# Optimization experiments

Hardware: AMD Instinct MI355X
Metric: run time of the kernel (lower is better)

Reference implementation:

```python
import jax, jax.numpy as jnp
import numpy as np

EPS = 1e-5

def _conv1x1(x, w, b=None):
    # x: (B, Cin, H, W), w: (Cout, Cin) -> (B, Cout, H, W)
    y = jnp.einsum('bchw,oc->bohw', x, w)
    if b is not None:
        y = y + b[None, :, None, None]
    return y

def setup_inputs() -> dict:
    key = jax.random.key(0)
    ks = jax.random.split(key, 14)
    B, C, I = 4, 256, 128
    Ha = Wa = 64
    Hd = Wd = 128
    s = 0.05
    return {
        'detect':  jax.random.normal(ks[0], (B, C, Hd, Wd), jnp.float32),
        'aim':     jax.random.normal(ks[1], (B, C, Ha, Wa), jnp.float32),
        'g_w':     jax.random.normal(ks[2], (I, C), jnp.float32) * s,
        'g_b':     jax.random.normal(ks[3], (I,), jnp.float32) * s,
        'theta_w': jax.random.normal(ks[4], (I, C), jnp.float32) * s,
        'theta_b': jax.random.normal(ks[5], (I,), jnp.float32) * s,
        'phi_w':   jax.random.normal(ks[6], (I, C), jnp.float32) * s,
        'phi_b':   jax.random.normal(ks[7], (I,), jnp.float32) * s,
        'q_w':     jax.random.normal(ks[8], (C, I), jnp.float32) * s,
        'q_b':     jax.random.normal(ks[9], (C,), jnp.float32) * s,
        'bn_gamma': jax.random.normal(ks[10], (C,), jnp.float32),
        'bn_beta':  jax.random.normal(ks[11], (C,), jnp.float32),
        'bn_mean':  jax.random.normal(ks[12], (C,), jnp.float32),
        'bn_var':   jax.random.uniform(ks[13], (C,), jnp.float32) + 0.5,
    }

def reference(detect, aim, g_w, g_b, theta_w, theta_b, phi_w, phi_b,
              q_w, q_b, bn_gamma, bn_beta, bn_mean, bn_var):
    B, C, Hd, Wd = detect.shape
    _, _, Ha, Wa = aim.shape
    Na = Ha * Wa
    Nd = Hd * Wd
    I = g_w.shape[0]

    # 1x1 conv projections, flattened to token sequences
    a_g   = _conv1x1(aim, g_w, g_b).reshape(B, I, Na)        # g(aim)
    th_a  = _conv1x1(aim, theta_w, theta_b).reshape(B, I, Na)
    ph_d  = _conv1x1(detect, phi_w, phi_b).reshape(B, I, Nd)
    # (d_x = g(detect) is dead code in the original forward; omitted)

    # f = theta_x @ phi_x : (B, Na, Nd); permuted -> (B, Nd, Na); N = Na
    f = jnp.einsum('bia,bid->bad', th_a, ph_d)               # (B, Na, Nd)
    inv_n = jnp.float32(1.0 / Na)
    # non_det = (f^T / Na) @ a_x : (B, Nd, I) -> permute -> (B, I, Nd)
    non = jnp.einsum('bad,bia->bid', f * inv_n, a_g)         # (B, I, Nd)
    non = non.reshape(B, I, Hd, Wd)

    # Q: 1x1 conv (I -> C) + BatchNorm (inference mode, running stats)
    y = _conv1x1(non, q_w, q_b)
    inv_std = jax.lax.rsqrt(bn_var + EPS)
    y = (y - bn_mean[None, :, None, None]) * (bn_gamma * inv_std)[None, :, None, None] \
        + bn_beta[None, :, None, None]

    return y + detect
```

## Files before the change

kernel.cpp:

```cpp
#include <hip/hip_runtime.h>

constexpr int BB   = 4;
constexpr int CCH  = 256;
constexpr int IDIM = 128;
constexpr int NAa  = 4096;
constexpr int NDd  = 16384;
constexpr int PAD  = 320;
constexpr float NAinv = 1.0f / 4096.0f;

typedef __bf16 bf16x8 __attribute__((ext_vector_type(8)));
typedef float  f32x4  __attribute__((ext_vector_type(4)));

__device__ inline unsigned short f2bfu(float f) {
    unsigned u = __float_as_uint(f);
    u += 0x7FFFu + ((u >> 16) & 1u);
    return (unsigned short)(u >> 16);
}

__global__ __launch_bounds__(256) void k_front(const float* __restrict__ aim,
                                               unsigned short* __restrict__ Abf,
                                               float* __restrict__ r,
                                               const float* __restrict__ qw,
                                               const float* __restrict__ gw,
                                               const float* __restrict__ gb,
                                               const float* __restrict__ thw,
                                               const float* __restrict__ thb,
                                               const float* __restrict__ phw,
                                               const float* __restrict__ phb,
                                               unsigned short* __restrict__ Ph,
                                               unsigned short* __restrict__ Rt) {
    __shared__ float red[256];
    const int t = threadIdx.x;
    if (blockIdx.x < BB * CCH) {
        const int row = blockIdx.x;
        const float* src = aim + (long)row * NAa;
        unsigned short* dst = Abf + (long)row * NAa;
        float s = 0.f;
        #pragma unroll
        for (int j = 0; j < 4; ++j) {
            const int e = (j * 256 + t) * 4;
            float4 v = *(const float4*)(src + e);
            s += v.x + v.y + v.z + v.w;
            ushort4 o; o.x = f2bfu(v.x); o.y = f2bfu(v.y); o.z = f2bfu(v.z); o.w = f2bfu(v.w);
            *(ushort4*)(dst + e) = o;
        }
        red[t] = s; __syncthreads();
        for (int st = 128; st > 0; st >>= 1) { if (t < st) red[t] += red[t + st]; __syncthreads(); }
        if (t == 0) r[row] = red[0];
    } else {
        const int idx = (blockIdx.x - BB * CCH) * 256 + t;
        if (idx < CCH * PAD) {
            const int o = idx / PAD, c = idx - o * PAD;
            float acc = 0.f;
            if (c <= 256) {
                for (int i = 0; i < IDIM; ++i)
                    acc += qw[o * IDIM + i] * ((c < 256) ? gw[i * CCH + c] : gb[i]);
            }
            Ph[idx] = f2bfu(acc);
        } else {
            const int id2 = idx - CCH * PAD;
            const int c2 = id2 / PAD, k = id2 - c2 * PAD;
            float acc = 0.f;
            if (k <= 256 && c2 <= 256) {
                for (int i = 0; i < IDIM; ++i) {
                    const float av = (k < 256) ? thw[i * CCH + k] : thb[i];
                    const float bv = (c2 < 256) ? phw[i * CCH + c2] : phb[i];
                    acc += av * bv;
                }
            }
            Rt[id2] = f2bfu(acc);
        }
    }
}

__global__ __launch_bounds__(64) void k_S(const unsigned short* __restrict__ Abf,
                                          float* __restrict__ Spart) {
    const int z = blockIdx.z, b = z >> 3, chunk = z & 7;
    const unsigned short* A = Abf + (long)b * CCH * NAa;
    const int lane = threadIdx.x, quad = lane >> 4, l16 = lane & 15;
    const int mb = blockIdx.y * 64, nb = blockIdx.x * 64;
    const int kb = chunk * 512;
    f32x4 acc[4][4] = {};
    for (int ks = 0; ks < 16; ++ks) {
        const int k = kb + ks * 32 + quad * 8;
        bf16x8 af[4], bfr[4];
        #pragma unroll
        for (int i = 0; i < 4; ++i) af[i]  = *(const bf16x8*)(A + (long)(mb + i * 16 + l16) * NAa + k);
        #pragma unroll
        for (int j = 0; j < 4; ++j) bfr[j] = *(const bf16x8*)(A + (long)(nb + j * 16 + l16) * NAa + k);
        #pragma unroll
        for (int i = 0; i < 4; ++i)
            #pragma unroll
            for (int j = 0; j < 4; ++j)
                acc[i][j] = __builtin_amdgcn_mfma_f32_16x16x32_bf16(af[i], bfr[j], acc[i][j], 0, 0, 0);
    }
    float* o = Spart + (long)z * CCH * CCH;
    #pragma unroll
    for (int i = 0; i < 4; ++i)
        #pragma unroll
        for (int j = 0; j < 4; ++j)
            #pragma unroll
            for (int reg = 0; reg < 4; ++reg)
                o[(long)(mb + i * 16 + quad * 4 + reg) * CCH + nb + j * 16 + l16] = acc[i][j][reg];
}

__global__ __launch_bounds__(256) void k_red(const float* __restrict__ Spart,
                                             const float* __restrict__ r,
                                             unsigned short* __restrict__ Shat) {
    const int b = blockIdx.y;
    const int idx = blockIdx.x * 256 + threadIdx.x;
    const int k = idx / PAD, n = idx - k * PAD;
    float v = 0.f;
    if (k < 256 && n < 256) {
        #pragma unroll
        for (int p = 0; p < 8; ++p)
            v += Spart[(long)(b * 8 + p) * CCH * CCH + k * CCH + n];
    } else if (k == 256 && n < 256) v = r[b * CCH + n];
    else if (n == 256 && k < 256)   v = r[b * CCH + k];
    else if (k == 256 && n == 256)  v = 4096.0f;
    Shat[(long)b * PAD * PAD + idx] = f2bfu(v);
}

__global__ __launch_bounds__(256) void k_t(const unsigned short* __restrict__ Ph,
                                           const unsigned short* __restrict__ Sh,
                                           const unsigned short* __restrict__ Rt,
                                           const float* __restrict__ qb,
                                           const float* __restrict__ gamma,
                                           const float* __restrict__ beta,
                                           const float* __restrict__ mean,
                                           const float* __restrict__ var,
                                           unsigned short* __restrict__ W5u,
                                           float* __restrict__ b5) {
    const int b = blockIdx.y;
    const int m0 = blockIdx.x * 64;
    const unsigned short* S = Sh + (long)b * PAD * PAD;
    const int t = threadIdx.x, w = t >> 6, lane = t & 63, quad = lane >> 4, l16 = lane & 15;
    __shared__ __align__(16) unsigned short Tl[64][328];

    {
        f32x4 a1[4][5] = {};
        for (int kt = 0; kt < PAD; kt += 32) {
            bf16x8 af[4], bfr[5];
            #pragma unroll
            for (int i = 0; i < 4; ++i)
                af[i] = *(const bf16x8*)(Ph + (long)(m0 + i * 16 + l16) * PAD + kt + quad * 8);
            #pragma unroll
            for (int j = 0; j < 5; ++j)
                bfr[j] = *(const bf16x8*)(S + (long)(w * 80 + j * 16 + l16) * PAD + kt + quad * 8);
            #pragma unroll
            for (int i = 0; i < 4; ++i)
                #pragma unroll
                for (int j = 0; j < 5; ++j)
                    a1[i][j] = __builtin_amdgcn_mfma_f32_16x16x32_bf16(af[i], bfr[j], a1[i][j], 0, 0, 0);
        }
        #pragma unroll
        for (int i = 0; i < 4; ++i)
            #pragma unroll
            for (int j = 0; j < 5; ++j)
                #pragma unroll
                for (int reg = 0; reg < 4; ++reg)
                    Tl[i * 16 + quad * 4 + reg][w * 80 + j * 16 + l16] = f2bfu(a1[i][j][reg]);
    }
    __syncthreads();

    for (int pass = 0; pass < 2; ++pass) {
        if (pass == 1 && w != 0) break;
        const int n0 = (pass == 0) ? w * 64 : 256;
        f32x4 acc[4][4] = {};
        for (int kt = 0; kt < PAD; kt += 32) {
            bf16x8 af[4], bfr[4];
            #pragma unroll
            for (int i = 0; i < 4; ++i)
                af[i] = *(const bf16x8*)&Tl[i * 16 + l16][kt + quad * 8];
            #pragma unroll
            for (int j = 0; j < 4; ++j)
                bfr[j] = *(const bf16x8*)(Rt + (long)(n0 + j * 16 + l16) * PAD + kt + quad * 8);
            #pragma unroll
            for (int i = 0; i < 4; ++i)
                #pragma unroll
                for (int j = 0; j < 4; ++j)
                    acc[i][j] = __builtin_amdgcn_mfma_f32_16x16x32_bf16(af[i], bfr[j], acc[i][j], 0, 0, 0);
        }
        #pragma unroll
        for (int i = 0; i < 4; ++i) {
            #pragma unroll
            for (int reg = 0; reg < 4; ++reg) {
                const int o = m0 + i * 16 + quad * 4 + reg;
                const float s = gamma[o] * rsqrtf(var[o] + 1e-5f);
                #pragma unroll
                for (int j = 0; j < 4; ++j) {
                    const int c2 = n0 + j * 16 + l16;
                    const float val = acc[i][j][reg] * s * NAinv;
                    if (c2 < CCH)
                        W5u[((long)b * CCH + o) * CCH + c2] = f2bfu(val + (o == c2 ? 1.0f : 0.0f));
                    else if (c2 == CCH)
                        b5[b * CCH + o] = val + s * (qb[o] - mean[o]) + beta[o];
                }
            }
        }
    }
}

__global__ __launch_bounds__(512) void k_final(const float* __restrict__ D0,
                                               const unsigned short* __restrict__ W5u,
                                               const float* __restrict__ b5,
                                               float* __restrict__ out) {
    const int z = blockIdx.z;
    const int nb = blockIdx.x * 128;
    const float* D = D0 + (long)z * CCH * NDd;
    float* O = out + (long)z * CCH * NDd;
    const unsigned short* W = W5u + (long)z * CCH * CCH;
    const int t = threadIdx.x, wv = t >> 6, lane = t & 63, quad = lane >> 4, l16 = lane & 15;
    const int mw = (wv >> 1) * 64, nw = (wv & 1) * 64;
    const int r2 = t >> 4, g = t & 15;
    const bool st = (t < 256);
    __shared__ __align__(16) unsigned short lb[2][128][40];

    f32x4 xa[4], xb[4];
    bf16x8 af[2][4], bfr[4];

    auto load_tile = [&](f32x4* x, int kt) {
        const float* base = D + (long)(kt + 2 * r2) * NDd + nb + 8 * g;
        x[0] = *(const f32x4*)(base);
        x[1] = *(const f32x4*)(base + NDd);
        x[2] = *(const f32x4*)(base + 4);
        x[3] = *(const f32x4*)(base + NDd + 4);
    };
    auto write_tile = [&](int buf, const f32x4* x) {
        #pragma unroll
        for (int e2 = 0; e2 < 2; ++e2)
            #pragma unroll
            for (int c = 0; c < 4; ++c) {
                const int n = 8 * g + 4 * e2 + c;
                const int p = ((n & 7) << 4) + (n >> 3);
                const unsigned v = (unsigned)f2bfu(x[2 * e2][c]) |
                                   ((unsigned)f2bfu(x[2 * e2 + 1][c]) << 16);
                *(unsigned*)&lb[buf][p][2 * r2] = v;
            }
    };
    auto loadW = [&](bf16x8* a, int kt) {
        #pragma unroll
        for (int i = 0; i < 4; ++i)
            a[i] = *(const bf16x8*)(W + (long)(mw + i * 16 + l16) * CCH + kt + quad * 8);
    };

    int pj[4];
    #pragma unroll
    for (int j = 0; j < 4; ++j) {
        const int n = nw + j * 16 + l16;
        pj[j] = ((n & 7) << 4) + (n >> 3);
    }

    f32x4 acc[4][4] = {};
    if (st) { load_tile(xa, 0); load_tile(xb, 32); }
    loadW(af[0], 0);
    if (st) { write_tile(0, xa); load_tile(xa, 64); }
    #pragma unroll
    for (int it = 0; it < 8; ++it) {
        __syncthreads();
        const int kt = it * 32;
        #pragma unroll
        for (int j = 0; j < 4; ++j)
            bfr[j] = *(const bf16x8*)&lb[it & 1][pj[j]][quad * 8];
        #pragma unroll
        for (int i = 0; i < 4; ++i)
            #pragma unroll
            for (int j = 0; j < 4; ++j)
                acc[i][j] = __builtin_amdgcn_mfma_f32_16x16x32_bf16(af[it & 1][i], bfr[j], acc[i][j], 0, 0, 0);
        if (it < 7) {
            loadW(af[(it + 1) & 1], kt + 32);
            if (st) {
                write_tile((it + 1) & 1, (it & 1) ? xa : xb);
                if (it < 5) load_tile((it & 1) ? xa : xb, (it + 3) * 32);
            }
        }
    }
    #pragma unroll
    for (int i = 0; i < 4; ++i) {
        float bv[4];
        #pragma unroll
        for (int reg = 0; reg < 4; ++reg)
            bv[reg] = b5[z * CCH + mw + i * 16 + quad * 4 + reg];
        #pragma unroll
        for (int j = 0; j < 4; ++j) {
            const int n = nb + nw + j * 16 + l16;
            #pragma unroll
            for (int reg = 0; reg < 4; ++reg)
                O[(long)(mw + i * 16 + quad * 4 + reg) * NDd + n] = acc[i][j][reg] + bv[reg];
        }
    }
}

extern "C" void kernel_launch(void* const* d_in, const int* in_sizes, int n_in,
                              void* d_out, int out_size, void* d_ws, size_t ws_size,
                              hipStream_t stream) {
    const float* detect = (const float*)d_in[0];
    const float* aim    = (const float*)d_in[1];
    const float* g_w    = (const float*)d_in[2];
    const float* g_b    = (const float*)d_in[3];
    const float* th_w   = (const float*)d_in[4];
    const float* th_b   = (const float*)d_in[5];
    const float* phi_w  = (const float*)d_in[6];
    const float* phi_b  = (const float*)d_in[7];
    const float* q_w    = (const float*)d_in[8];
    const float* q_b    = (const float*)d_in[9];
    const float* gamma  = (const float*)d_in[10];
    const float* beta   = (const float*)d_in[11];
    const float* mean   = (const float*)d_in[12];
    const float* var    = (const float*)d_in[13];
    float* out = (float*)d_out;

    float* ws = (float*)d_ws;
    unsigned short* Abf = (unsigned short*)ws;
    float* r     = ws + 2097152;
    float* Spart = r + 1024;
    unsigned short* ub = (unsigned short*)(Spart + 2097152);
    unsigned short* Shat_u  = ub;
    unsigned short* Phat_u  = Shat_u + 409600;
    unsigned short* RhatT_u = Phat_u + 81920;
    unsigned short* That_u  = RhatT_u + 102400;
    unsigned short* W5u     = That_u + 327680;
    float* b5 = (float*)(W5u + 262144);

    k_front<<<dim3(BB * CCH + (CCH * PAD + PAD * PAD) / 256), dim3(256), 0, stream>>>(
        aim, Abf, r, q_w, g_w, g_b, th_w, th_b, phi_w, phi_b, Phat_u, RhatT_u);
    k_S<<<dim3(4, 4, BB * 8), dim3(64), 0, stream>>>(Abf, Spart);
    k_red<<<dim3(PAD * PAD / 256, BB), dim3(256), 0, stream>>>(Spart, r, Shat_u);
    k_t<<<dim3(4, BB), dim3(256), 0, stream>>>(Phat_u, Shat_u, RhatT_u, q_b, gamma, beta, mean, var, W5u, b5);
    k_final<<<dim3(NDd / 128, 1, BB), dim3(512), 0, stream>>>(detect, W5u, b5, out);
}
```

Baseline: 228.7 us.

## Fuse all stages into one cooperative persistent kernel with grid syncs

Replaces the five separate launches with a single cooperative kernel of 512 blocks that runs every stage and separates them with grid-wide barriers, removing per-launch overhead and gaps between kernels. The S-partial GEMM now splits its K range across 8 waves per block and reduces them through shared memory. The T and W5 GEMMs are retiled into 80 single-wave tiles. Grid syncs cost something, and the small GEMM stages now use only one wave in a subset of blocks, so those stages may run slower than before.

Result: slower. 252.9 us (+10.6%).

```diff
diff --git a/kernel.cpp b/kernel.cpp
--- a/kernel.cpp
+++ b/kernel.cpp
@@ -1,4 +1,7 @@
 #include <hip/hip_runtime.h>
+#include <hip/hip_cooperative_groups.h>
+
+namespace cg = cooperative_groups;
 
 constexpr int BB   = 4;
 constexpr int CCH  = 256;
@@ -17,276 +20,316 @@
     return (unsigned short)(u >> 16);
 }
 
-__global__ __launch_bounds__(256) void k_front(const float* __restrict__ aim,
-                                               unsigned short* __restrict__ Abf,
-                                               float* __restrict__ r,
-                                               const float* __restrict__ qw,
-                                               const float* __restrict__ gw,
-                                               const float* __restrict__ gb,
-                                               const float* __restrict__ thw,
-                                               const float* __restrict__ thb,
-                                               const float* __restrict__ phw,
-                                               const float* __restrict__ phb,
-                                               unsigned short* __restrict__ Ph,
-                                               unsigned short* __restrict__ Rt) {
-    __shared__ float red[256];
-    const int t = threadIdx.x;
-    if (blockIdx.x < BB * CCH) {
-        const int row = blockIdx.x;
-        const float* src = aim + (long)row * NAa;
-        unsigned short* dst = Abf + (long)row * NAa;
-        float s = 0.f;
+struct Par {
+    const float* aim; const float* qw; const float* gw; const float* gb;
+    const float* thw; const float* thb; const float* phw; const float* phb;
+    const float* qb; const float* gamma; const float* beta; const float* mean; const float* var;
+    const float* detect; float* out;
+    unsigned short* Abf; float* r; float* Spart;
+    unsigned short* Shat; unsigned short* Ph; unsigned short* Rt; unsigned short* Th; unsigned short* W5;
+    float* b5;
+};
+
+template<int PHASE> __device__ inline void gsync() {
+    if constexpr (PHASE < 0) cg::this_grid().sync();
+}
+
+template<int PHASE>
+__global__ __launch_bounds__(512, 4) void k_mega(Par p) {
+    __shared__ __align__(16) char smraw[32768];
+    const int bid = blockIdx.x, t = threadIdx.x;
+    const int wv = t >> 6, lane = t & 63, quad = lane >> 4, l16 = lane & 15;
+
+    if (PHASE < 0 || PHASE == 0) {
+        {
+            const int half = t >> 8, tt = t & 255;
+            const int row = bid * 2 + half;
+            const float* src = p.aim + (long)row * NAa;
+            unsigned short* dst = p.Abf + (long)row * NAa;
+            float s = 0.f;
+            #pragma unroll
+            for (int j = 0; j < 4; ++j) {
+                const int e = (j * 256 + tt) * 4;
+                float4 v = *(const float4*)(src + e);
+                s += v.x + v.y + v.z + v.w;
+                ushort4 o; o.x = f2bfu(v.x); o.y = f2bfu(v.y); o.z = f2bfu(v.z); o.w = f2bfu(v.w);
+                *(ushort4*)(dst + e) = o;
+            }
+            float* red = (float*)smraw;
+            red[t] = s; __syncthreads();
+            for (int st_ = 128; st_ > 0; st_ >>= 1) {
+                if (tt < st_) red[half * 256 + tt] += red[half * 256 + tt + st_];
+                __syncthreads();
+            }
+            if (tt == 0) p.r[row] = red[half * 256];
+        }
+        {
+            const int idx = bid * 512 + t;
+            if (idx < CCH * PAD) {
+                const int o = idx / PAD, c = idx - o * PAD;
+                float acc = 0.f;
+                if (c <= 256) {
+                    for (int i = 0; i < IDIM; ++i)
+                        acc += p.qw[o * IDIM + i] * ((c < 256) ? p.gw[i * CCH + c] : p.gb[i]);
+                }
+                p.Ph[idx] = f2bfu(acc);
+            } else if (idx < CCH * PAD + PAD * PAD) {
+                const int id2 = idx - CCH * PAD;
+                const int c2 = id2 / PAD, k = id2 - c2 * PAD;
+                float acc = 0.f;
+                if (k <= 256 && c2 <= 256) {
+                    for (int i = 0; i < IDIM; ++i) {
+                        const float av = (k < 256) ? p.thw[i * CCH + k] : p.thb[i];
+                        const float bv = (c2 < 256) ? p.phw[i * CCH + c2] : p.phb[i];
+                        acc += av * bv;
+                    }
+                }
+                p.Rt[id2] = f2bfu(acc);
+            }
+        }
+    }
+    gsync<PHASE>();
+
+    if (PHASE < 0 || PHASE == 1) {
+        const int z = bid >> 4, rem = bid & 15;
+        const int b = z >> 3;
+        const unsigned short* A = p.Abf + (long)b * CCH * NAa;
+        const int mb = (rem >> 2) * 64, nbb = (rem & 3) * 64;
+        const int kb = (z & 7) * 512;
+        f32x4 acc[4][4] = {};
+        #pragma unroll
+        for (int s = 0; s < 2; ++s) {
+            const int k = kb + (wv * 2 + s) * 32 + quad * 8;
+            bf16x8 af[4], bfr[4];
+            #pragma unroll
+            for (int i = 0; i < 4; ++i) af[i]  = *(const bf16x8*)(A + (long)(mb + i * 16 + l16) * NAa + k);
+            #pragma unroll
+            for (int j = 0; j < 4; ++j) bfr[j] = *(const bf16x8*)(A + (long)(nbb + j * 16 + l16) * NAa + k);
+            #pragma unroll
+            for (int i = 0; i < 4; ++i)
+                #pragma unroll
+                for (int j = 0; j < 4; ++j)
+                    acc[i][j] = __builtin_amdgcn_mfma_f32_16x16x32_bf16(af[i], bfr[j], acc[i][j], 0, 0, 0);
+        }
+        float* sred = (float*)smraw;
+        auto lput = [&](int rg) {
+            #pragma unroll
+            for (int i = 0; i < 4; ++i)
+                #pragma unroll
+                for (int j = 0; j < 4; ++j)
+                    #pragma unroll
+                    for (int rr = 0; rr < 4; ++rr)
+                        sred[rg * 4096 + ((i * 4 + j) * 4 + rr) * 64 + lane] = acc[i][j][rr];
+        };
+        auto ladd = [&](int rg) {
+            #pragma unroll
+            for (int i = 0; i < 4; ++i)
+                #pragma unroll
+                for (int j = 0; j < 4; ++j)
+                    #pragma unroll
+                    for (int rr = 0; rr < 4; ++rr)
+                        acc[i][j][rr] += sred[rg * 4096 + ((i * 4 + j) * 4 + rr) * 64 + lane];
+        };
+        if (wv == 4 || wv == 5) lput(wv - 4);
+        __syncthreads();
+        if (wv == 0 || wv == 1) ladd(wv);
+        __syncthreads();
+        if (wv == 6 || wv == 7) lput(wv - 6);
+        __syncthreads();
+        if (wv == 2 || wv == 3) ladd(wv - 2);
+        __syncthreads();
+        if (wv == 2 || wv == 3) lput(wv - 2);
+        __syncthreads();
+        if (wv == 0 || wv == 1) ladd(wv);
+        __syncthreads();
+        if (wv == 1) lput(0);
+        __syncthreads();
+        if (wv == 0) {
+            ladd(0);
+            float* o = p.Spart + (long)z * CCH * CCH;
+            #pragma unroll
+            for (int i = 0; i < 4; ++i)
+                #pragma unroll
+                for (int j = 0; j < 4; ++j)
+                    #pragma unroll
+                    for (int reg = 0; reg < 4; ++reg)
+                        o[(long)(mb + i * 16 + quad * 4 + reg) * CCH + nbb + j * 16 + l16] = acc[i][j][reg];
+        }
+    }
+    gsync<PHASE>();
+
+    if (PHASE < 0 || PHASE == 2) {
+        for (int e = bid * 512 + t; e < BB * PAD * PAD; e += 512 * 512) {
+            const int b = e / (PAD * PAD), idx = e - b * (PAD * PAD);
+            const int k = idx / PAD, n = idx - k * PAD;
+            float v = 0.f;
+            if (k < 256 && n < 256) {
+                #pragma unroll
+                for (int pp = 0; pp < 8; ++pp)
+                    v += p.Spart[(long)(b * 8 + pp) * CCH * CCH + k * CCH + n];
+            } else if (k == 256 && n < 256) v = p.r[b * CCH + n];
+            else if (n == 256 && k < 256)   v = p.r[b * CCH + k];
+            else if (k == 256 && n == 256)  v = 4096.0f;
+            p.Shat[(long)b * PAD * PAD + idx] = f2bfu(v);
+        }
+    }
+    gsync<PHASE>();
+
+    if (PHASE < 0 || PHASE == 3) {
+        if (wv == 0 && (bid % 6) == 0 && (bid / 6) < 80) {
+            const int tid = bid / 6;
+            const int b = tid / 20, rem2 = tid % 20;
+            const int n0 = (rem2 % 5) * 64, m0 = (rem2 / 5) * 64;
+            const unsigned short* S = p.Shat + (long)b * PAD * PAD;
+            unsigned short* T = p.Th + (long)b * CCH * PAD;
+            f32x4 acc[4][4] = {};
+            for (int kt = 0; kt < PAD; kt += 32) {
+                bf16x8 af[4], bfr[4];
+                #pragma unroll
+                for (int i = 0; i < 4; ++i) af[i]  = *(const bf16x8*)(p.Ph + (long)(m0 + i * 16 + l16) * PAD + kt + quad * 8);
+                #pragma unroll
+                for (int j = 0; j < 4; ++j) bfr[j] = *(const bf16x8*)(S + (long)(n0 + j * 16 + l16) * PAD + kt + quad * 8);
+                #pragma unroll
+                for (int i = 0; i < 4; ++i)
+                    #pragma unroll
+                    for (int j = 0; j < 4; ++j)
+                        acc[i][j] = __builtin_amdgcn_mfma_f32_16x16x32_bf16(af[i], bfr[j], acc[i][j], 0, 0, 0);
+            }
+            #pragma unroll
+            for (int i = 0; i < 4; ++i)
+                #pragma unroll
+                for (int j = 0; j < 4; ++j)
+                    #pragma unroll
+                    for (int reg = 0; reg < 4; ++reg)
+                        T[(long)(m0 + i * 16 + quad * 4 + reg) * PAD + n0 + j * 16 + l16] = f2bfu(acc[i][j][reg]);
+        }
+    }
+    gsync<PHASE>();
+
+    if (PHASE < 0 || PHASE == 4) {
+        if (wv == 0 && (bid % 6) == 0 && (bid / 6) < 80) {
+            const int tid = bid / 6;
+            const int b = tid / 20, rem2 = tid % 20;
+            const int n0 = (rem2 % 5) * 64, m0 = (rem2 / 5) * 64;
+            const unsigned short* A = p.Th + (long)b * CCH * PAD;
+            f32x4 acc[4][4] = {};
+            for (int kt = 0; kt < PAD; kt += 32) {
+                bf16x8 af[4], bfr[4];
+                #pragma unroll
+                for (int i = 0; i < 4; ++i) af[i]  = *(const bf16x8*)(A + (long)(m0 + i * 16 + l16) * PAD + kt + quad * 8);
+                #pragma unroll
+                for (int j = 0; j < 4; ++j) bfr[j] = *(const bf16x8*)(p.Rt + (long)(n0 + j * 16 + l16) * PAD + kt + quad * 8);
+                #pragma unroll
+                for (int i = 0; i < 4; ++i)
+                    #pragma unroll
+                    for (int j = 0; j < 4; ++j)
+                        acc[i][j] = __builtin_amdgcn_mfma_f32_16x16x32_bf16(af[i], bfr[j], acc[i][j], 0, 0, 0);
+            }
+            #pragma unroll
+            for (int i = 0; i < 4; ++i) {
+                #pragma unroll
+                for (int reg = 0; reg < 4; ++reg) {
+                    const int o = m0 + i * 16 + quad * 4 + reg;
+                    const float s = p.gamma[o] * rsqrtf(p.var[o] + 1e-5f);
+                    #pragma unroll
+                    for (int j = 0; j < 4; ++j) {
+                        const int c2 = n0 + j * 16 + l16;
+                        const float val = acc[i][j][reg] * s * NAinv;
+                        if (c2 < CCH)
+                            p.W5[((long)b * CCH + o) * CCH + c2] = f2bfu(val + (o == c2 ? 1.0f : 0.0f));
+                        else if (c2 == CCH)
+                            p.b5[b * CCH + o] = val + s * (p.qb[o] - p.mean[o]) + p.beta[o];
+                    }
+                }
+            }
+        }
+    }
+    gsync<PHASE>();
+
+    if (PHASE < 0 || PHASE == 5) {
+        const int z = bid >> 7;
+        const int nb = (bid & 127) * 128;
+        const float* D = p.detect + (long)z * CCH * NDd;
+        float* O = p.out + (long)z * CCH * NDd;
+        const unsigned short* W = p.W5 + (long)z * CCH * CCH;
+        const int mw = (wv >> 1) * 64, nw = (wv & 1) * 64;
+        const int r2 = t >> 4, g = t & 15;
+        const bool st = (t < 256);
+        auto lb = (unsigned short (*)[128][40])smraw;
+
+        f32x4 xa[4], xb[4];
+        bf16x8 af2[2][4], bfr[4];
+
+        auto load_tile = [&](f32x4* x, int kt) {
+            const float* base = D + (long)(kt + 2 * r2) * NDd + nb + 8 * g;
+            x[0] = *(const f32x4*)(base);
+            x[1] = *(const f32x4*)(base + NDd);
+            x[2] = *(const f32x4*)(base + 4);
+            x[3] = *(const f32x4*)(base + NDd + 4);
+        };
+        auto write_tile = [&](int buf, const f32x4* x) {
+            #pragma unroll
+            for (int e2 = 0; e2 < 2; ++e2)
+                #pragma unroll
+                for (int c = 0; c < 4; ++c) {
+                    const int n = 8 * g + 4 * e2 + c;
+                    const int pp = ((n & 7) << 4) + (n >> 3);
+                    const unsigned v = (unsigned)f2bfu(x[2 * e2][c]) |
+                                       ((unsigned)f2bfu(x[2 * e2 + 1][c]) << 16);
+                    *(unsigned*)&lb[buf][pp][2 * r2] = v;
+                }
+        };
+        auto loadW = [&](bf16x8* a, int kt) {
+            #pragma unroll
+            for (int i = 0; i < 4; ++i)
+                a[i] = *(const bf16x8*)(W + (long)(mw + i * 16 + l16) * CCH + kt + quad * 8);
+        };
+
+        int pj[4];
         #pragma unroll
         for (int j = 0; j < 4; ++j) {
-            const int e = (j * 256 + t) * 4;
-            float4 v = *(const float4*)(src + e);
-            s += v.x + v.y + v.z + v.w;
-            ushort4 o; o.x = f2bfu(v.x); o.y = f2bfu(v.y); o.z = f2bfu(v.z); o.w = f2bfu(v.w);
-            *(ushort4*)(dst + e) = o;
-        }
-        red[t] = s; __syncthreads();
-        for (int st = 128; st > 0; st >>= 1) { if (t < st) red[t] += red[t + st]; __syncthreads(); }
-        if (t == 0) r[row] = red[0];
-    } else {
-        const int idx = (blockIdx.x - BB * CCH) * 256 + t;
-        if (idx < CCH * PAD) {
-            const int o = idx / PAD, c = idx - o * PAD;
-            float acc = 0.f;
-            if (c <= 256) {
-                for (int i = 0; i < IDIM; ++i)
-                    acc += qw[o * IDIM + i] * ((c < 256) ? gw[i * CCH + c] : gb[i]);
-            }
-            Ph[idx] = f2bfu(acc);
-        } else {
-            const int id2 = idx - CCH * PAD;
-            const int c2 = id2 / PAD, k = id2 - c2 * PAD;
-            float acc = 0.f;
-            if (k <= 256 && c2 <= 256) {
-                for (int i = 0; i < IDIM; ++i) {
-                    const float av = (k < 256) ? thw[i * CCH + k] : thb[i];
-                    const float bv = (c2 < 256) ? phw[i * CCH + c2] : phb[i];
-                    acc += av * bv;
-                }
-            }
-            Rt[id2] = f2bfu(acc);
-        }
-    }
-}
-
-__global__ __launch_bounds__(64) void k_S(const unsigned short* __restrict__ Abf,
-                                          float* __restrict__ Spart) {
-    const int z = blockIdx.z, b = z >> 3, chunk = z & 7;
-    const unsigned short* A = Abf + (long)b * CCH * NAa;
-    const int lane = threadIdx.x, quad = lane >> 4, l16 = lane & 15;
-    const int mb = blockIdx.y * 64, nb = blockIdx.x * 64;
-    const int kb = chunk * 512;
-    f32x4 acc[4][4] = {};
-    for (int ks = 0; ks < 16; ++ks) {
-        const int k = kb + ks * 32 + quad * 8;
-        bf16x8 af[4], bfr[4];
+            const int n = nw + j * 16 + l16;
+            pj[j] = ((n & 7) << 4) + (n >> 3);
+        }
+
+        f32x4 acc[4][4] = {};
+        __syncthreads();
+        if (st) { load_tile(xa, 0); load_tile(xb, 32); }
+        loadW(af2[0], 0);
+        if (st) { write_tile(0, xa); load_tile(xa, 64); }
         #pragma unroll
-        for (int i = 0; i < 4; ++i) af[i]  = *(const bf16x8*)(A + (long)(mb + i * 16 + l16) * NAa + k);
-        #pragma unroll
-        for (int j = 0; j < 4; ++j) bfr[j] = *(const bf16x8*)(A + (long)(nb + j * 16 + l16) * NAa + k);
-        #pragma unroll
-        for (int i = 0; i < 4; ++i)
+        for (int it = 0; it < 8; ++it) {
+            __syncthreads();
+            const int kt = it * 32;
             #pragma unroll
             for (int j = 0; j < 4; ++j)
-                acc[i][j] = __builtin_amdgcn_mfma_f32_16x16x32_bf16(af[i], bfr[j], acc[i][j], 0, 0, 0);
-    }
-    float* o = Spart + (long)z * CCH * CCH;
-    #pragma unroll
-    for (int i = 0; i < 4; ++i)
-        #pragma unroll
-        for (int j = 0; j < 4; ++j)
-            #pragma unroll
-            for (int reg = 0; reg < 4; ++reg)
-                o[(long)(mb + i * 16 + quad * 4 + reg) * CCH + nb + j * 16 + l16] = acc[i][j][reg];
-}
-
-__global__ __launch_bounds__(256) void k_red(const float* __restrict__ Spart,
-                                             const float* __restrict__ r,
-                                             unsigned short* __restrict__ Shat) {
-    const int b = blockIdx.y;
-    const int idx = blockIdx.x * 256 + threadIdx.x;
-    const int k = idx / PAD, n = idx - k * PAD;
-    float v = 0.f;
-    if (k < 256 && n < 256) {
-        #pragma unroll
-        for (int p = 0; p < 8; ++p)
-            v += Spart[(long)(b * 8 + p) * CCH * CCH + k * CCH + n];
-    } else if (k == 256 && n < 256) v = r[b * CCH + n];
-    else if (n == 256 && k < 256)   v = r[b * CCH + k];
-    else if (k == 256 && n == 256)  v = 4096.0f;
-    Shat[(long)b * PAD * PAD + idx] = f2bfu(v);
-}
-
-__global__ __launch_bounds__(256) void k_t(const unsigned short* __restrict__ Ph,
-                                           const unsigned short* __restrict__ Sh,
-                                           const unsigned short* __restrict__ Rt,
-                                           const float* __restrict__ qb,
-                                           const float* __restrict__ gamma,
-                                           const float* __restrict__ beta,
-                                           const float* __restrict__ mean,
-                                           const float* __restrict__ var,
-                                           unsigned short* __restrict__ W5u,
-                                           float* __restrict__ b5) {
-    const int b = blockIdx.y;
-    const int m0 = blockIdx.x * 64;
-    const unsigned short* S = Sh + (long)b * PAD * PAD;
-    const int t = threadIdx.x, w = t >> 6, lane = t & 63, quad = lane >> 4, l16 = lane & 15;
-    __shared__ __align__(16) unsigned short Tl[64][328];
-
-    {
-        f32x4 a1[4][5] = {};
-        for (int kt = 0; kt < PAD; kt += 32) {
-            bf16x8 af[4], bfr[5];
-            #pragma unroll
-            for (int i = 0; i < 4; ++i)
-                af[i] = *(const bf16x8*)(Ph + (long)(m0 + i * 16 + l16) * PAD + kt + quad * 8);
-            #pragma unroll
-            for (int j = 0; j < 5; ++j)
-                bfr[j] = *(const bf16x8*)(S + (long)(w * 80 + j * 16 + l16) * PAD + kt + quad * 8);
-            #pragma unroll
-            for (int i = 0; i < 4; ++i)
-                #pragma unroll
-                for (int j = 0; j < 5; ++j)
-                    a1[i][j] = __builtin_amdgcn_mfma_f32_16x16x32_bf16(af[i], bfr[j], a1[i][j], 0, 0, 0);
-        }
-        #pragma unroll
-        for (int i = 0; i < 4; ++i)
-            #pragma unroll
-            for (int j = 0; j < 5; ++j)
-                #pragma unroll
-                for (int reg = 0; reg < 4; ++reg)
-                    Tl[i * 16 + quad * 4 + reg][w * 80 + j * 16 + l16] = f2bfu(a1[i][j][reg]);
-    }
-    __syncthreads();
-
-    for (int pass = 0; pass < 2; ++pass) {
-        if (pass == 1 && w != 0) break;
-        const int n0 = (pass == 0) ? w * 64 : 256;
-        f32x4 acc[4][4] = {};
-        for (int kt = 0; kt < PAD; kt += 32) {
-            bf16x8 af[4], bfr[4];
-            #pragma unroll
-            for (int i = 0; i < 4; ++i)
-                af[i] = *(const bf16x8*)&Tl[i * 16 + l16][kt + quad * 8];
-            #pragma unroll
-            for (int j = 0; j < 4; ++j)
-                bfr[j] = *(const bf16x8*)(Rt + (long)(n0 + j * 16 + l16) * PAD + kt + quad * 8);
-            #pragma unroll
-            for (int i = 0; i < 4; ++i)
-                #pragma unroll
-                for (int j = 0; j < 4; ++j)
-                    acc[i][j] = __builtin_amdgcn_mfma_f32_16x16x32_bf16(af[i], bfr[j], acc[i][j], 0, 0, 0);
+                bfr[j] = *(const bf16x8*)&lb[it & 1][pj[j]][quad * 8];
+            #pragma unroll
+            for (int i = 0; i < 4; ++i)
+                #pragma unroll
+                for (int j = 0; j < 4; ++j)
+                    acc[i][j] = __builtin_amdgcn_mfma_f32_16x16x32_bf16(af2[it & 1][i], bfr[j], acc[i][j], 0, 0, 0);
+            if (it < 7) {
+                loadW(af2[(it + 1) & 1], kt + 32);
+                if (st) {
+                    write_tile((it + 1) & 1, (it & 1) ? xa : xb);
+                    if (it < 5) load_tile((it & 1) ? xa : xb, (it + 3) * 32);
+                }
+            }
         }
         #pragma unroll
         for (int i = 0; i < 4; ++i) {
-            #pragma unroll
-            for (int reg = 0; reg < 4; ++reg) {
-                const int o = m0 + i * 16 + quad * 4 + reg;
-                const float s = gamma[o] * rsqrtf(var[o] + 1e-5f);
-                #pragma unroll
-                for (int j = 0; j < 4; ++j) {
-                    const int c2 = n0 + j * 16 + l16;
-                    const float val = acc[i][j][reg] * s * NAinv;
-                    if (c2 < CCH)
-                        W5u[((long)b * CCH + o) * CCH + c2] = f2bfu(val + (o == c2 ? 1.0f : 0.0f));
-                    else if (c2 == CCH)
-                        b5[b * CCH + o] = val + s * (qb[o] - mean[o]) + beta[o];
-                }
-            }
-        }
-    }
-}
-
-__global__ __launch_bounds__(512) void k_final(const float* __restrict__ D0,
-                                               const unsigned short* __restrict__ W5u,
-                                               const float* __restrict__ b5,
-                                               float* __restrict__ out) {
-    const int z = blockIdx.z;
-    const int nb = blockIdx.x * 128;
-    const float* D = D0 + (long)z * CCH * NDd;
-    float* O = out + (long)z * CCH * NDd;
-    const unsigned short* W = W5u + (long)z * CCH * CCH;
-    const int t = threadIdx.x, wv = t >> 6, lane = t & 63, quad = lane >> 4, l16 = lane & 15;
-    const int mw = (wv >> 1) * 64, nw = (wv & 1) * 64;
-    const int r2 = t >> 4, g = t & 15;
-    const bool st = (t < 256);
-    __shared__ __align__(16) unsigned short lb[2][128][40];
-
-    f32x4 xa[4], xb[4];
-    bf16x8 af[2][4], bfr[4];
-
-    auto load_tile = [&](f32x4* x, int kt) {
-        const float* base = D + (long)(kt + 2 * r2) * NDd + nb + 8 * g;
-        x[0] = *(const f32x4*)(base);
-        x[1] = *(const f32x4*)(base + NDd);
-        x[2] = *(const f32x4*)(base + 4);
-        x[3] = *(const f32x4*)(base + NDd + 4);
-    };
-    auto write_tile = [&](int buf, const f32x4* x) {
-        #pragma unroll
-        for (int e2 = 0; e2 < 2; ++e2)
-            #pragma unroll
-            for (int c = 0; c < 4; ++c) {
-                const int n = 8 * g + 4 * e2 + c;
-                const int p = ((n & 7) << 4) + (n >> 3);
-                const unsigned v = (unsigned)f2bfu(x[2 * e2][c]) |
-                                   ((unsigned)f2bfu(x[2 * e2 + 1][c]) << 16);
-                *(unsigned*)&lb[buf][p][2 * r2] = v;
-            }
-    };
-    auto loadW = [&](bf16x8* a, int kt) {
-        #pragma unroll
-        for (int i = 0; i < 4; ++i)
-            a[i] = *(const bf16x8*)(W + (long)(mw + i * 16 + l16) * CCH + kt + quad * 8);
-    };
-
-    int pj[4];
-    #pragma unroll
-    for (int j = 0; j < 4; ++j) {
-        const int n = nw + j * 16 + l16;
-        pj[j] = ((n & 7) << 4) + (n >> 3);
-    }
-
-    f32x4 acc[4][4] = {};
-    if (st) { load_tile(xa, 0); load_tile(xb, 32); }
-    loadW(af[0], 0);
-    if (st) { write_tile(0, xa); load_tile(xa, 64); }
-    #pragma unroll
-    for (int it = 0; it < 8; ++it) {
-        __syncthreads();
-        const int kt = it * 32;
-        #pragma unroll
-        for (int j = 0; j < 4; ++j)
-            bfr[j] = *(const bf16x8*)&lb[it & 1][pj[j]][quad * 8];
-        #pragma unroll
-        for (int i = 0; i < 4; ++i)
-            #pragma unroll
-            for (int j = 0; j < 4; ++j)
-                acc[i][j] = __builtin_amdgcn_mfma_f32_16x16x32_bf16(af[it & 1][i], bfr[j], acc[i][j], 0, 0, 0);
-        if (it < 7) {
-            loadW(af[(it + 1) & 1], kt + 32);
-            if (st) {
-                write_tile((it + 1) & 1, (it & 1) ? xa : xb);
-                if (it < 5) load_tile((it & 1) ? xa : xb, (it + 3) * 32);
-            }
-        }
-    }
-    #pragma unroll
-    for (int i = 0; i < 4; ++i) {
-        float bv[4];
-        #pragma unroll
-        for (int reg = 0; reg < 4; ++reg)
-            bv[reg] = b5[z * CCH + mw + i * 16 + quad * 4 + reg];
-        #pragma unroll
-        for (int j = 0; j < 4; ++j) {
-            const int n = nb + nw + j * 16 + l16;
+            float bv[4];
             #pragma unroll
             for (int reg = 0; reg < 4; ++reg)
-                O[(long)(mw + i * 16 + quad * 4 + reg) * NDd + n] = acc[i][j][reg] + bv[reg];
+                bv[reg] = p.b5[z * CCH + mw + i * 16 + quad * 4 + reg];
+            #pragma unroll
+            for (int j = 0; j < 4; ++j) {
+                const int n = nb + nw + j * 16 + l16;
+                #pragma unroll
+                for (int reg = 0; reg < 4; ++reg)
+                    O[(long)(mw + i * 16 + quad * 4 + reg) * NDd + n] = acc[i][j][reg] + bv[reg];
+            }
         }
     }
 }
@@ -294,22 +337,6 @@
 extern "C" void kernel_launch(void* const* d_in, const int* in_sizes, int n_in,
                               void* d_out, int out_size, void* d_ws, size_t ws_size,
                               hipStream_t stream) {
-    const float* detect = (const float*)d_in[0];
-    const float* aim    = (const float*)d_in[1];
-    const float* g_w    = (const float*)d_in[2];
-    const float* g_b    = (const float*)d_in[3];
-    const float* th_w   = (const float*)d_in[4];
-    const float* th_b   = (const float*)d_in[5];
-    const float* phi_w  = (const float*)d_in[6];
-    const float* phi_b  = (const float*)d_in[7];
-    const float* q_w    = (const float*)d_in[8];
-    const float* q_b    = (const float*)d_in[9];
-    const float* gamma  = (const float*)d_in[10];
-    const float* beta   = (const float*)d_in[11];
-    const float* mean   = (const float*)d_in[12];
-    const float* var    = (const float*)d_in[13];
-    float* out = (float*)d_out;
-
     float* ws = (float*)d_ws;
     unsigned short* Abf = (unsigned short*)ws;
     float* r     = ws + 2097152;
@@ -322,10 +349,40 @@
     unsigned short* W5u     = That_u + 327680;
     float* b5 = (float*)(W5u + 262144);
 
-    k_front<<<dim3(BB * CCH + (CCH * PAD + PAD * PAD) / 256), dim3(256), 0, stream>>>(
-        aim, Abf, r, q_w, g_w, g_b, th_w, th_b, phi_w, phi_b, Phat_u, RhatT_u);
-    k_S<<<dim3(4, 4, BB * 8), dim3(64), 0, stream>>>(Abf, Spart);
-    k_red<<<dim3(PAD * PAD / 256, BB), dim3(256), 0, stream>>>(Spart, r, Shat_u);
-    k_t<<<dim3(4, BB), dim3(256), 0, stream>>>(Phat_u, Shat_u, RhatT_u, q_b, gamma, beta, mean, var, W5u, b5);
-    k_final<<<dim3(NDd / 128, 1, BB), dim3(512), 0, stream>>>(detect, W5u, b5, out);
+    Par pp;
+    pp.aim    = (const float*)d_in[1];
+    pp.qw     = (const float*)d_in[8];
+    pp.gw     = (const float*)d_in[2];
+    pp.gb     = (const float*)d_in[3];
+    pp.thw    = (const float*)d_in[4];
+    pp.thb    = (const float*)d_in[5];
+    pp.phw    = (const float*)d_in[6];
+    pp.phb    = (const float*)d_in[7];
+    pp.qb     = (const float*)d_in[9];
+    pp.gamma  = (const float*)d_in[10];
+    pp.beta   = (const float*)d_in[11];
+    pp.mean   = (const float*)d_in[12];
+    pp.var    = (const float*)d_in[13];
+    pp.detect = (const float*)d_in[0];
+    pp.out    = (float*)d_out;
+    pp.Abf = Abf; pp.r = r; pp.Spart = Spart;
+    pp.Shat = Shat_u; pp.Ph = Phat_u; pp.Rt = RhatT_u; pp.Th = That_u; pp.W5 = W5u;
+    pp.b5 = b5;
+
+    static int occ = -1;
+    if (occ < 0) {
+        if (hipOccupancyMaxActiveBlocksPerMultiprocessor(&occ, k_mega<-1>, 512, 0) != hipSuccess)
+            occ = 0;
+    }
+    if (occ >= 2) {
+        void* args[] = { (void*)&pp };
+        hipLaunchCooperativeKernel(k_mega<-1>, dim3(512), dim3(512), args, 0, stream);
+    } else {
+        k_mega<0><<<dim3(512), dim3(512), 0, stream>>>(pp);
+        k_mega<1><<<dim3(512), dim3(512), 0, stream>>>(pp);
+        k_mega<2><<<dim3(512), dim3(512), 0, stream>>>(pp);
+        k_mega<3><<<dim3(512), dim3(512), 0, stream>>>(pp);
+        k_mega<4><<<dim3(512), dim3(512), 0, stream>>>(pp);
+        k_mega<5><<<dim3(512), dim3(512), 0, stream>>>(pp);
+    }
 }
```

## Reassociate weight-folding chain: project aim tokens first, then reduce over tokens

Applied to the files above, without the earlier changes.

Replaces the Gram-matrix path (aim·aimᵀ split-K partials, reduction kernel, then two small GEMMs) with a different association order. A new kernel stages a 64-token tile of aim in swizzled LDS as bf16 and multiplies it by the folded Q·g and θᵀφ matrices, giving projected token tensors V1/V2. A second kernel contracts V1 and V2 over the 4096 tokens with an in-block split-K reduction through shared memory to form the folded weight W5 and bias. This removes the Spart buffer round-trip and one launch, at the cost of writing and reading larger intermediate V tensors and doing more MFMA work for the projections.

Result: slower. 240.2 us (+5.0%).

```diff
diff --git a/kernel.cpp b/kernel.cpp
--- a/kernel.cpp
+++ b/kernel.cpp
@@ -17,113 +17,99 @@
     return (unsigned short)(u >> 16);
 }
 
-__global__ __launch_bounds__(256) void k_front(const float* __restrict__ aim,
-                                               unsigned short* __restrict__ Abf,
-                                               float* __restrict__ r,
-                                               const float* __restrict__ qw,
-                                               const float* __restrict__ gw,
-                                               const float* __restrict__ gb,
-                                               const float* __restrict__ thw,
-                                               const float* __restrict__ thb,
-                                               const float* __restrict__ phw,
-                                               const float* __restrict__ phb,
-                                               unsigned short* __restrict__ Ph,
-                                               unsigned short* __restrict__ Rt) {
-    __shared__ float red[256];
-    const int t = threadIdx.x;
-    if (blockIdx.x < BB * CCH) {
-        const int row = blockIdx.x;
-        const float* src = aim + (long)row * NAa;
-        unsigned short* dst = Abf + (long)row * NAa;
-        float s = 0.f;
-        #pragma unroll
-        for (int j = 0; j < 4; ++j) {
-            const int e = (j * 256 + t) * 4;
-            float4 v = *(const float4*)(src + e);
-            s += v.x + v.y + v.z + v.w;
-            ushort4 o; o.x = f2bfu(v.x); o.y = f2bfu(v.y); o.z = f2bfu(v.z); o.w = f2bfu(v.w);
-            *(ushort4*)(dst + e) = o;
-        }
-        red[t] = s; __syncthreads();
-        for (int st = 128; st > 0; st >>= 1) { if (t < st) red[t] += red[t + st]; __syncthreads(); }
-        if (t == 0) r[row] = red[0];
+__global__ __launch_bounds__(256) void k_prep(const float* __restrict__ qw,
+                                              const float* __restrict__ gw,
+                                              const float* __restrict__ gb,
+                                              const float* __restrict__ thw,
+                                              const float* __restrict__ thb,
+                                              const float* __restrict__ phw,
+                                              const float* __restrict__ phb,
+                                              unsigned short* __restrict__ Ph,
+                                              unsigned short* __restrict__ Rt) {
+    const int idx = blockIdx.x * 256 + threadIdx.x;
+    if (idx < CCH * PAD) {
+        const int o = idx / PAD, c = idx - o * PAD;
+        float acc = 0.f;
+        if (c <= 256) {
+            for (int i = 0; i < IDIM; ++i)
+                acc += qw[o * IDIM + i] * ((c < 256) ? gw[i * CCH + c] : gb[i]);
+        }
+        Ph[idx] = f2bfu(acc);
     } else {
-        const int idx = (blockIdx.x - BB * CCH) * 256 + t;
-        if (idx < CCH * PAD) {
-            const int o = idx / PAD, c = idx - o * PAD;
-            float acc = 0.f;
-            if (c <= 256) {
-                for (int i = 0; i < IDIM; ++i)
-                    acc += qw[o * IDIM + i] * ((c < 256) ? gw[i * CCH + c] : gb[i]);
+        const int id2 = idx - CCH * PAD;
+        const int c2 = id2 / PAD, k = id2 - c2 * PAD;
+        float acc = 0.f;
+        if (k <= 256 && c2 <= 256) {
+            for (int i = 0; i < IDIM; ++i) {
+                const float av = (k < 256) ? thw[i * CCH + k] : thb[i];
+                const float bv = (c2 < 256) ? phw[i * CCH + c2] : phb[i];
+                acc += av * bv;
             }
-            Ph[idx] = f2bfu(acc);
-        } else {
-            const int id2 = idx - CCH * PAD;
-            const int c2 = id2 / PAD, k = id2 - c2 * PAD;
-            float acc = 0.f;
-            if (k <= 256 && c2 <= 256) {
-                for (int i = 0; i < IDIM; ++i) {
-                    const float av = (k < 256) ? thw[i * CCH + k] : thb[i];
-                    const float bv = (c2 < 256) ? phw[i * CCH + c2] : phb[i];
-                    acc += av * bv;
-                }
-            }
-            Rt[id2] = f2bfu(acc);
-        }
-    }
-}
-
-__global__ __launch_bounds__(64) void k_S(const unsigned short* __restrict__ Abf,
-                                          float* __restrict__ Spart) {
-    const int z = blockIdx.z, b = z >> 3, chunk = z & 7;
-    const unsigned short* A = Abf + (long)b * CCH * NAa;
-    const int lane = threadIdx.x, quad = lane >> 4, l16 = lane & 15;
-    const int mb = blockIdx.y * 64, nb = blockIdx.x * 64;
-    const int kb = chunk * 512;
-    f32x4 acc[4][4] = {};
-    for (int ks = 0; ks < 16; ++ks) {
-        const int k = kb + ks * 32 + quad * 8;
-        bf16x8 af[4], bfr[4];
-        #pragma unroll
-        for (int i = 0; i < 4; ++i) af[i]  = *(const bf16x8*)(A + (long)(mb + i * 16 + l16) * NAa + k);
-        #pragma unroll
-        for (int j = 0; j < 4; ++j) bfr[j] = *(const bf16x8*)(A + (long)(nb + j * 16 + l16) * NAa + k);
-        #pragma unroll
-        for (int i = 0; i < 4; ++i)
-            #pragma unroll
-            for (int j = 0; j < 4; ++j)
-                acc[i][j] = __builtin_amdgcn_mfma_f32_16x16x32_bf16(af[i], bfr[j], acc[i][j], 0, 0, 0);
-    }
-    float* o = Spart + (long)z * CCH * CCH;
-    #pragma unroll
-    for (int i = 0; i < 4; ++i)
-        #pragma unroll
-        for (int j = 0; j < 4; ++j)
-            #pragma unroll
-            for (int reg = 0; reg < 4; ++reg)
-                o[(long)(mb + i * 16 + quad * 4 + reg) * CCH + nb + j * 16 + l16] = acc[i][j][reg];
-}
-
-__global__ __launch_bounds__(256) void k_red(const float* __restrict__ Spart,
-                                             const float* __restrict__ r,
-                                             unsigned short* __restrict__ Shat) {
-    const int b = blockIdx.y;
-    const int idx = blockIdx.x * 256 + threadIdx.x;
-    const int k = idx / PAD, n = idx - k * PAD;
-    float v = 0.f;
-    if (k < 256 && n < 256) {
-        #pragma unroll
-        for (int p = 0; p < 8; ++p)
-            v += Spart[(long)(b * 8 + p) * CCH * CCH + k * CCH + n];
-    } else if (k == 256 && n < 256) v = r[b * CCH + n];
-    else if (n == 256 && k < 256)   v = r[b * CCH + k];
-    else if (k == 256 && n == 256)  v = 4096.0f;
-    Shat[(long)b * PAD * PAD + idx] = f2bfu(v);
-}
-
-__global__ __launch_bounds__(256) void k_t(const unsigned short* __restrict__ Ph,
-                                           const unsigned short* __restrict__ Sh,
+        }
+        Rt[id2] = f2bfu(acc);
+    }
+}
+
+__device__ inline int at_idx(int row, int col) {
+    return row * 320 + ((((col >> 3) ^ (row & 7)) << 3) | (col & 7));
+}
+
+__global__ __launch_bounds__(256) void k_V(const float* __restrict__ aim,
+                                           const unsigned short* __restrict__ Ph,
                                            const unsigned short* __restrict__ Rt,
+                                           unsigned short* __restrict__ V1,
+                                           unsigned short* __restrict__ V2) {
+    const int b = blockIdx.y, n0 = blockIdx.x * 64;
+    const float* A = aim + (long)b * CCH * NAa;
+    const int t = threadIdx.x, w = t >> 6, lane = t & 63, quad = lane >> 4, l16 = lane & 15;
+    __shared__ __align__(16) unsigned short At[64 * 320];
+
+    #pragma unroll 4
+    for (int rep = 0; rep < 64; ++rep) {
+        const int c = rep * 4 + w;
+        At[at_idx(lane, c)] = f2bfu(A[(long)c * NAa + n0 + lane]);
+    }
+    {
+        const int nn = t & 63, k0 = 256 + (t >> 6) * 16;
+        #pragma unroll
+        for (int k = k0; k < k0 + 16; ++k)
+            At[at_idx(nn, k)] = (k == 256) ? (unsigned short)0x3F80u : (unsigned short)0u;
+    }
+    __syncthreads();
+
+    for (int task = w; task < 9; task += 4) {
+        const unsigned short* src;
+        unsigned short* dst;
+        int m0;
+        if (task < 4) { m0 = task * 64;       src = Ph; dst = V1 + (long)b * CCH * NAa; }
+        else          { m0 = (task - 4) * 64; src = Rt; dst = V2 + (long)b * PAD * NAa; }
+        f32x4 acc[4][4] = {};
+        for (int kt = 0; kt < PAD; kt += 32) {
+            bf16x8 af[4], bfr[4];
+            #pragma unroll
+            for (int i = 0; i < 4; ++i)
+                af[i] = *(const bf16x8*)(src + (long)(m0 + i * 16 + l16) * PAD + kt + quad * 8);
+            #pragma unroll
+            for (int j = 0; j < 4; ++j)
+                bfr[j] = *(const bf16x8*)&At[at_idx(j * 16 + l16, kt + quad * 8)];
+            #pragma unroll
+            for (int i = 0; i < 4; ++i)
+                #pragma unroll
+                for (int j = 0; j < 4; ++j)
+                    acc[i][j] = __builtin_amdgcn_mfma_f32_16x16x32_bf16(af[i], bfr[j], acc[i][j], 0, 0, 0);
+        }
+        #pragma unroll
+        for (int i = 0; i < 4; ++i)
+            #pragma unroll
+            for (int j = 0; j < 4; ++j)
+                #pragma unroll
+                for (int reg = 0; reg < 4; ++reg)
+                    dst[(long)(m0 + i * 16 + quad * 4 + reg) * NAa + n0 + j * 16 + l16] = f2bfu(acc[i][j][reg]);
+    }
+}
+
+__global__ __launch_bounds__(256) void k_W(const unsigned short* __restrict__ V1,
+                                           const unsigned short* __restrict__ V2,
                                            const float* __restrict__ qb,
                                            const float* __restrict__ gamma,
                                            const float* __restrict__ beta,
@@ -131,56 +117,50 @@
                                            const float* __restrict__ var,
                                            unsigned short* __restrict__ W5u,
                                            float* __restrict__ b5) {
-    const int b = blockIdx.y;
-    const int m0 = blockIdx.x * 64;
-    const unsigned short* S = Sh + (long)b * PAD * PAD;
+    const int b = blockIdx.z;
+    const int n0 = blockIdx.x * 64, m0 = blockIdx.y * 64;
+    const unsigned short* Va = V1 + (long)b * CCH * NAa;
+    const unsigned short* Vb = V2 + (long)b * PAD * NAa;
     const int t = threadIdx.x, w = t >> 6, lane = t & 63, quad = lane >> 4, l16 = lane & 15;
-    __shared__ __align__(16) unsigned short Tl[64][328];
-
-    {
-        f32x4 a1[4][5] = {};
-        for (int kt = 0; kt < PAD; kt += 32) {
-            bf16x8 af[4], bfr[5];
-            #pragma unroll
-            for (int i = 0; i < 4; ++i)
-                af[i] = *(const bf16x8*)(Ph + (long)(m0 + i * 16 + l16) * PAD + kt + quad * 8);
-            #pragma unroll
-            for (int j = 0; j < 5; ++j)
-                bfr[j] = *(const bf16x8*)(S + (long)(w * 80 + j * 16 + l16) * PAD + kt + quad * 8);
-            #pragma unroll
-            for (int i = 0; i < 4; ++i)
-                #pragma unroll
-                for (int j = 0; j < 5; ++j)
-                    a1[i][j] = __builtin_amdgcn_mfma_f32_16x16x32_bf16(af[i], bfr[j], a1[i][j], 0, 0, 0);
-        }
-        #pragma unroll
-        for (int i = 0; i < 4; ++i)
-            #pragma unroll
-            for (int j = 0; j < 5; ++j)
+    __shared__ float sred[3 * 4096];
+
+    f32x4 acc[4][4] = {};
+    for (int ks = 0; ks < 32; ++ks) {
+        const int k = w * 1024 + ks * 32 + quad * 8;
+        bf16x8 af[4], bfr[4];
+        #pragma unroll
+        for (int i = 0; i < 4; ++i) af[i]  = *(const bf16x8*)(Va + (long)(m0 + i * 16 + l16) * NAa + k);
+        #pragma unroll
+        for (int j = 0; j < 4; ++j) bfr[j] = *(const bf16x8*)(Vb + (long)(n0 + j * 16 + l16) * NAa + k);
+        #pragma unroll
+        for (int i = 0; i < 4; ++i)
+            #pragma unroll
+            for (int j = 0; j < 4; ++j)
+                acc[i][j] = __builtin_amdgcn_mfma_f32_16x16x32_bf16(af[i], bfr[j], acc[i][j], 0, 0, 0);
+    }
+    if (w > 0) {
+        #pragma unroll
+        for (int i = 0; i < 4; ++i)
+            #pragma unroll
+            for (int j = 0; j < 4; ++j)
                 #pragma unroll
                 for (int reg = 0; reg < 4; ++reg)
-                    Tl[i * 16 + quad * 4 + reg][w * 80 + j * 16 + l16] = f2bfu(a1[i][j][reg]);
+                    sred[(w - 1) * 4096 + ((i * 4 + j) * 4 + reg) * 64 + lane] = acc[i][j][reg];
     }
     __syncthreads();
-
-    for (int pass = 0; pass < 2; ++pass) {
-        if (pass == 1 && w != 0) break;
-        const int n0 = (pass == 0) ? w * 64 : 256;
-        f32x4 acc[4][4] = {};
-        for (int kt = 0; kt < PAD; kt += 32) {
-            bf16x8 af[4], bfr[4];
-            #pragma unroll
-            for (int i = 0; i < 4; ++i)
-                af[i] = *(const bf16x8*)&Tl[i * 16 + l16][kt + quad * 8];
-            #pragma unroll
-            for (int j = 0; j < 4; ++j)
-                bfr[j] = *(const bf16x8*)(Rt + (long)(n0 + j * 16 + l16) * PAD + kt + quad * 8);
-            #pragma unroll
-            for (int i = 0; i < 4; ++i)
-                #pragma unroll
-                for (int j = 0; j < 4; ++j)
-                    acc[i][j] = __builtin_amdgcn_mfma_f32_16x16x32_bf16(af[i], bfr[j], acc[i][j], 0, 0, 0);
-        }
+    if (w == 0) {
+        #pragma unroll
+        for (int i = 0; i < 4; ++i)
+            #pragma unroll
+            for (int j = 0; j < 4; ++j)
+                #pragma unroll
+                for (int reg = 0; reg < 4; ++reg) {
+                    float v = acc[i][j][reg];
+                    #pragma unroll
+                    for (int rg = 0; rg < 3; ++rg)
+                        v += sred[rg * 4096 + ((i * 4 + j) * 4 + reg) * 64 + lane];
+                    acc[i][j][reg] = v;
+                }
         #pragma unroll
         for (int i = 0; i < 4; ++i) {
             #pragma unroll
@@ -310,22 +290,17 @@
     const float* var    = (const float*)d_in[13];
     float* out = (float*)d_out;
 
-    float* ws = (float*)d_ws;
-    unsigned short* Abf = (unsigned short*)ws;
-    float* r     = ws + 2097152;
-    float* Spart = r + 1024;
-    unsigned short* ub = (unsigned short*)(Spart + 2097152);
-    unsigned short* Shat_u  = ub;
-    unsigned short* Phat_u  = Shat_u + 409600;
+    unsigned short* us = (unsigned short*)d_ws;
+    unsigned short* V1u = us;
+    unsigned short* V2u = V1u + 4194304;
+    unsigned short* Phat_u  = V2u + 5242880;
     unsigned short* RhatT_u = Phat_u + 81920;
-    unsigned short* That_u  = RhatT_u + 102400;
-    unsigned short* W5u     = That_u + 327680;
+    unsigned short* W5u     = RhatT_u + 102400;
     float* b5 = (float*)(W5u + 262144);
 
-    k_front<<<dim3(BB * CCH + (CCH * PAD + PAD * PAD) / 256), dim3(256), 0, stream>>>(
-        aim, Abf, r, q_w, g_w, g_b, th_w, th_b, phi_w, phi_b, Phat_u, RhatT_u);
-    k_S<<<dim3(4, 4, BB * 8), dim3(64), 0, stream>>>(Abf, Spart);
-    k_red<<<dim3(PAD * PAD / 256, BB), dim3(256), 0, stream>>>(Spart, r, Shat_u);
-    k_t<<<dim3(4, BB), dim3(256), 0, stream>>>(Phat_u, Shat_u, RhatT_u, q_b, gamma, beta, mean, var, W5u, b5);
+    k_prep<<<dim3((CCH * PAD + PAD * PAD) / 256), dim3(256), 0, stream>>>(
+        q_w, g_w, g_b, th_w, th_b, phi_w, phi_b, Phat_u, RhatT_u);
+    k_V<<<dim3(NAa / 64, BB), dim3(256), 0, stream>>>(aim, Phat_u, RhatT_u, V1u, V2u);
+    k_W<<<dim3(5, 4, BB), dim3(256), 0, stream>>>(V1u, V2u, q_b, gamma, beta, mean, var, W5u, b5);
     k_final<<<dim3(NDd / 128, 1, BB), dim3(512), 0, stream>>>(detect, W5u, b5, out);
 }
```
